# Optimization experiments

Measured on AMD Instinct MI355X. Metric: run time of the kernel, lower is better.

Reference implementation:

```python
import jax, jax.numpy as jnp
import numpy as np
from jax import lax

B, L = 4, 512
D_MODEL, D_STATE, D_CONV, EXPAND = 1024, 16, 4, 2
D_INNER = EXPAND * D_MODEL
DT_RANK = (D_MODEL + 15) // 16  # math.ceil(d_model / 16) = 64


def setup_inputs() -> dict:
    key = jax.random.key(0)
    ks = jax.random.split(key, 16)

    def rn(k, shape, scale=1.0):
        return jax.random.normal(k, shape, jnp.float32) * scale

    # A initialized as log(1..d_state) broadcast over d_inner, as in the module
    A_log = jnp.log(jnp.broadcast_to(jnp.arange(1, D_STATE + 1, dtype=jnp.float32), (D_INNER, D_STATE)))
    return {
        "hidden_states": rn(ks[0], (B, L, D_MODEL)),
        "in_proj_w": rn(ks[1], (2 * D_INNER, D_MODEL), D_MODEL ** -0.5),
        "conv1d_w": rn(ks[2], (D_INNER, 1, D_CONV), D_CONV ** -0.5),
        "conv1d_bias": rn(ks[3], (D_INNER,), 0.02),
        "x_proj_w": rn(ks[4], (DT_RANK + 2 * D_STATE, D_INNER), D_INNER ** -0.5),
        "dt_proj_w": rn(ks[5], (D_INNER, DT_RANK), DT_RANK ** -0.5),
        "dt_proj_bias": rn(ks[6], (D_INNER,), 0.02) - 4.0,
        "A_log": A_log,
        "D": jnp.ones((D_INNER,), jnp.float32),
        "conv1d_b_w": rn(ks[7], (D_INNER, 1, D_CONV), D_CONV ** -0.5),
        "conv1d_b_bias": rn(ks[8], (D_INNER,), 0.02),
        "x_proj_b_w": rn(ks[9], (DT_RANK + 2 * D_STATE, D_INNER), D_INNER ** -0.5),
        "dt_proj_b_w": rn(ks[10], (D_INNER, DT_RANK), DT_RANK ** -0.5),
        "dt_proj_b_bias": rn(ks[11], (D_INNER,), 0.02) - 4.0,
        "A_b_log": A_log,
        "D_b": jnp.ones((D_INNER,), jnp.float32),
        "out_proj_w": rn(ks[12], (D_MODEL, D_INNER), D_INNER ** -0.5),
    }


def _selective_scan(u, delta, A, Bm, Cm, Dv):
    # u, delta: [b,l,d]; Bm, Cm: [b,l,n]; A: [d,n]; Dv: [d]
    # h_t = exp(delta_t * A) * h_{t-1} + delta_t * B_t * u_t ; y_t = <h_t, C_t> + D * u_t
    def step(h, inp):
        u_t, dt_t, B_t, C_t = inp  # [b,d], [b,d], [b,n], [b,n]
        dA = jnp.exp(dt_t[:, :, None] * A)  # [b,d,n]
        h = dA * h + (dt_t * u_t)[:, :, None] * B_t[:, None, :]
        y = jnp.einsum('bdn,bn->bd', h, C_t)
        return h, y

    b, l, d = u.shape
    h0 = jnp.zeros((b, d, A.shape[1]), u.dtype)
    xs = (u.transpose(1, 0, 2), delta.transpose(1, 0, 2), Bm.transpose(1, 0, 2), Cm.transpose(1, 0, 2))
    _, ys = lax.scan(step, h0, xs)  # ys: [l,b,d]
    return ys.transpose(1, 0, 2) + u * Dv


def _direction(x_bdl, conv_w, conv_b, xproj_w, dtproj_w, dtproj_b, A_log, Dv):
    # x_bdl: [b, d_inner, l]. torch pads both sides with d_conv-1 then slices [:L] -> causal depthwise conv.
    xc = lax.conv_general_dilated(x_bdl, conv_w, (1,), [(D_CONV - 1, 0)],
                                  dimension_numbers=('NCH', 'OIH', 'NCH'),
                                  feature_group_count=D_INNER)
    xc = (xc + conv_b[None, :, None]).transpose(0, 2, 1)  # [b,l,d_inner]
    x_dbl = xc @ xproj_w.T  # [b,l,dt_rank+2n]
    dt = x_dbl[..., :DT_RANK] @ dtproj_w.T + dtproj_b
    Bm = x_dbl[..., DT_RANK:DT_RANK + D_STATE]
    Cm = x_dbl[..., DT_RANK + D_STATE:]
    xc = jnp.clip(xc, -10.0, 10.0)
    dt = jnp.clip(dt, 1e-5, 1.0)
    # source passes dt_proj.bias again as delta_bias with delta_softplus=True (bias added twice; faithful)
    delta = jax.nn.softplus(dt + dtproj_b)
    A = -jnp.exp(A_log)
    return _selective_scan(xc, delta, A, Bm, Cm, Dv)


def reference(hidden_states, in_proj_w, conv1d_w, conv1d_bias, x_proj_w, dt_proj_w, dt_proj_bias,
              A_log, D, conv1d_b_w, conv1d_b_bias, x_proj_b_w, dt_proj_b_w, dt_proj_b_bias,
              A_b_log, D_b, out_proj_w):
    xz = (hidden_states @ in_proj_w.T).transpose(0, 2, 1)  # [b, 2*d_inner, l]
    x, z = jnp.split(xz, 2, axis=1)  # each [b, d_inner, l]
    y_fwd = _direction(x, conv1d_w, conv1d_bias, x_proj_w, dt_proj_w, dt_proj_bias, A_log, D)
    y_bwd = _direction(x[:, :, ::-1], conv1d_b_w, conv1d_b_bias, x_proj_b_w, dt_proj_b_w,
                       dt_proj_b_bias, A_b_log, D_b)[:, ::-1, :]  # flip back along seq
    y = (y_fwd + y_bwd) * jax.nn.silu(z.transpose(0, 2, 1))  # [b,l,d_inner]
    out = y @ out_proj_w.T  # [b,l,d_model]
    return jnp.nan_to_num(out, nan=0.0, posinf=1.0, neginf=-1.0)
```

## Files before the change

kernel.cpp:

```cpp
#include <hip/hip_runtime.h>
#include <hip/hip_bf16.h>
#include <math.h>

#define BB 4
#define LL 512
#define DMODEL 1024
#define DSTATE 16
#define DCONV 4
#define DINNER 2048
#define DTRANK 64
#define MROWS (BB*LL)
#define G2KS 4
#define SCHUNK 32
#define SNC (LL / SCHUNK)

typedef __hip_bfloat16 bf16;
typedef __attribute__((ext_vector_type(8))) short short8;
typedef __attribute__((ext_vector_type(4))) short short4v;
typedef __attribute__((ext_vector_type(4))) float f32x4;

__device__ __forceinline__ float softplusf(float x) {
    return x > 20.f ? x : log1pf(__expf(x));
}

__device__ __forceinline__ void stage16(const void* g, void* l) {
    __builtin_amdgcn_global_load_lds(
        (const __attribute__((address_space(1))) void*)g,
        (__attribute__((address_space(3))) void*)l, 16, 0, 0);
}

__device__ __forceinline__ bool a_is_arange(const float* Aa) {
    bool ok = true;
#pragma unroll
    for (int n = 1; n < DSTATE; ++n) {
        float k = (float)(n + 1);
        ok = ok && (fabsf(Aa[n] - k * Aa[0]) <= 1e-4f * k * fabsf(Aa[0]));
    }
    return ok;
}

template<int EPI>
__global__ __launch_bounds__(256) void gemm_bf16(
    const bf16* __restrict__ A, const bf16* __restrict__ W,
    float* __restrict__ C, int N, int K, int lda, int ldw, int ldc)
{
    __shared__ bf16 lA[128 * 32];
    __shared__ bf16 lW[128 * 32];

    const int tid = threadIdx.x;
    const int lane = tid & 63;
    const int wid = tid >> 6;
    const int wr = wid >> 1;
    const int wc = wid & 1;
    const int rowBase = blockIdx.y * 128;
    const int colBase = blockIdx.x * 128;

    const int r16 = lane & 15;
    const int kg = lane >> 4;

    const int srow = (lane >> 2);
    const int scol = (lane & 3) * 8;

    f32x4 acc[4][4];
#pragma unroll
    for (int m = 0; m < 4; ++m)
#pragma unroll
        for (int n = 0; n < 4; ++n) acc[m][n] = (f32x4)0.f;

    for (int k0 = 0; k0 < K; k0 += 32) {
#pragma unroll
        for (int c = 0; c < 2; ++c) {
            int r = wid * 32 + c * 16 + srow;
            stage16(&A[(size_t)(rowBase + r) * lda + k0 + scol],
                    &lA[(wid * 32 + c * 16) * 32]);
            stage16(&W[(size_t)(colBase + r) * ldw + k0 + scol],
                    &lW[(wid * 32 + c * 16) * 32]);
        }
        __syncthreads();

        short8 a[4], b[4];
#pragma unroll
        for (int m = 0; m < 4; ++m)
            a[m] = *(const short8*)&lA[(wr * 64 + m * 16 + r16) * 32 + kg * 8];
#pragma unroll
        for (int n = 0; n < 4; ++n)
            b[n] = *(const short8*)&lW[(wc * 64 + n * 16 + r16) * 32 + kg * 8];
#pragma unroll
        for (int m = 0; m < 4; ++m)
#pragma unroll
            for (int n = 0; n < 4; ++n)
                acc[m][n] = __builtin_amdgcn_mfma_f32_16x16x32_bf16(
                    a[m], b[n], acc[m][n], 0, 0, 0);
        __syncthreads();
    }

#pragma unroll
    for (int m = 0; m < 4; ++m) {
#pragma unroll
        for (int n = 0; n < 4; ++n) {
            int gc = colBase + wc * 64 + n * 16 + r16;
#pragma unroll
            for (int j = 0; j < 4; ++j) {
                int gr = rowBase + wr * 64 + m * 16 + kg * 4 + j;
                float v = acc[m][n][j];
                if (EPI == 2) {
                    if (isnan(v)) v = 0.f;
                    else if (isinf(v)) v = (v > 0.f) ? 1.f : -1.f;
                }
                C[(size_t)gr * ldc + gc] = v;
            }
        }
    }
}

__global__ __launch_bounds__(256) void g4_mfma(
    const bf16* __restrict__ A, const bf16* __restrict__ W,
    float* __restrict__ part)
{
    const int kz = blockIdx.z;
    const int kOff = kz * 1024;
    float* C = part + (size_t)kz * 2048 * 1024;

    __shared__ bf16 lA[128 * 32];
    __shared__ bf16 lW[128 * 32];

    const int tid = threadIdx.x;
    const int lane = tid & 63;
    const int wid = tid >> 6;
    const int wr = wid >> 1;
    const int wc = wid & 1;
    const int rowBase = blockIdx.y * 128;
    const int colBase = blockIdx.x * 128;

    const int r16 = lane & 15;
    const int kg = lane >> 4;
    const int srow = (lane >> 2);
    const int scol = (lane & 3) * 8;

    f32x4 acc[4][4];
#pragma unroll
    for (int m = 0; m < 4; ++m)
#pragma unroll
        for (int n = 0; n < 4; ++n) acc[m][n] = (f32x4)0.f;

    for (int k0 = 0; k0 < 1024; k0 += 32) {
#pragma unroll
        for (int c = 0; c < 2; ++c) {
            int r = wid * 32 + c * 16 + srow;
            stage16(&A[(size_t)(rowBase + r) * 2048 + kOff + k0 + scol],
                    &lA[(wid * 32 + c * 16) * 32]);
            stage16(&W[(size_t)(colBase + r) * 2048 + kOff + k0 + scol],
                    &lW[(wid * 32 + c * 16) * 32]);
        }
        __syncthreads();

        short8 a[4], b[4];
#pragma unroll
        for (int m = 0; m < 4; ++m)
            a[m] = *(const short8*)&lA[(wr * 64 + m * 16 + r16) * 32 + kg * 8];
#pragma unroll
        for (int n = 0; n < 4; ++n)
            b[n] = *(const short8*)&lW[(wc * 64 + n * 16 + r16) * 32 + kg * 8];
#pragma unroll
        for (int m = 0; m < 4; ++m)
#pragma unroll
            for (int n = 0; n < 4; ++n)
                acc[m][n] = __builtin_amdgcn_mfma_f32_16x16x32_bf16(
                    a[m], b[n], acc[m][n], 0, 0, 0);
        __syncthreads();
    }

#pragma unroll
    for (int m = 0; m < 4; ++m) {
#pragma unroll
        for (int n = 0; n < 4; ++n) {
            int gc = colBase + wc * 64 + n * 16 + r16;
#pragma unroll
            for (int j = 0; j < 4; ++j) {
                int gr = rowBase + wr * 64 + m * 16 + kg * 4 + j;
                C[(size_t)gr * 1024 + gc] = acc[m][n][j];
            }
        }
    }
}

__global__ __launch_bounds__(256) void g4_reduce(
    const float* __restrict__ part, float* __restrict__ out)
{
    int i = (blockIdx.x * 256 + threadIdx.x) * 4;
    float4 p0 = *(const float4*)&part[i];
    float4 p1 = *(const float4*)&part[2048 * 1024 + i];
    float r[4] = { p0.x + p1.x, p0.y + p1.y, p0.z + p1.z, p0.w + p1.w };
#pragma unroll
    for (int j = 0; j < 4; ++j) {
        float v = r[j];
        if (isnan(v)) v = 0.f;
        else if (isinf(v)) v = (v > 0.f) ? 1.f : -1.f;
        r[j] = v;
    }
    *(float4*)&out[i] = *(float4*)r;
}

__global__ __launch_bounds__(256) void g3_mfma(
    const bf16* __restrict__ xdbl_bf,
    const bf16* __restrict__ dtw_bf,
    const float* __restrict__ biasf, const float* __restrict__ biasb,
    float* __restrict__ of, float* __restrict__ ob)
{
    const int dir = blockIdx.z;
    const bf16* A = xdbl_bf + (size_t)dir * 2048 * 96;
    const bf16* W = dtw_bf + (size_t)dir * 2048 * 64;
    const float* bias = dir ? biasb : biasf;
    float* C = dir ? ob : of;

    __shared__ bf16 lA[128 * 32];
    __shared__ bf16 lW[128 * 32];

    const int tid = threadIdx.x;
    const int lane = tid & 63;
    const int wid = tid >> 6;
    const int wr = wid >> 1;
    const int wc = wid & 1;
    const int rowBase = blockIdx.y * 128;
    const int colBase = blockIdx.x * 128;

    const int r16 = lane & 15;
    const int kg = lane >> 4;
    const int srow = (lane >> 2);
    const int scol = (lane & 3) * 8;

    f32x4 acc[4][4];
#pragma unroll
    for (int m = 0; m < 4; ++m)
#pragma unroll
        for (int n = 0; n < 4; ++n) acc[m][n] = (f32x4)0.f;

#pragma unroll
    for (int k0 = 0; k0 < 64; k0 += 32) {
#pragma unroll
        for (int c = 0; c < 2; ++c) {
            int r = wid * 32 + c * 16 + srow;
            stage16(&A[(size_t)(rowBase + r) * 96 + k0 + scol],
                    &lA[(wid * 32 + c * 16) * 32]);
            stage16(&W[(size_t)(colBase + r) * 64 + k0 + scol],
                    &lW[(wid * 32 + c * 16) * 32]);
        }
        __syncthreads();

        short8 a[4], b[4];
#pragma unroll
        for (int m = 0; m < 4; ++m)
            a[m] = *(const short8*)&lA[(wr * 64 + m * 16 + r16) * 32 + kg * 8];
#pragma unroll
        for (int n = 0; n < 4; ++n)
            b[n] = *(const short8*)&lW[(wc * 64 + n * 16 + r16) * 32 + kg * 8];
#pragma unroll
        for (int m = 0; m < 4; ++m)
#pragma unroll
            for (int n = 0; n < 4; ++n)
                acc[m][n] = __builtin_amdgcn_mfma_f32_16x16x32_bf16(
                    a[m], b[n], acc[m][n], 0, 0, 0);
        __syncthreads();
    }

#pragma unroll
    for (int m = 0; m < 4; ++m) {
#pragma unroll
        for (int n = 0; n < 4; ++n) {
            int gc = colBase + wc * 64 + n * 16 + r16;
            float bv = bias[gc];
#pragma unroll
            for (int j = 0; j < 4; ++j) {
                int gr = rowBase + wr * 64 + m * 16 + kg * 4 + j;
                float t = acc[m][n][j] + bv;
                t = fminf(fmaxf(t, 1e-5f), 1.0f);
                C[(size_t)gr * 2048 + gc] = softplusf(t + bv);
            }
        }
    }
}

__global__ __launch_bounds__(256) void g2_mfma(
    const bf16* __restrict__ xcbf_f, const bf16* __restrict__ xcbf_b,
    const bf16* __restrict__ wxf, const bf16* __restrict__ wxb,
    float* __restrict__ part)
{
    const int dir = blockIdx.z;
    const bf16* A = dir ? xcbf_b : xcbf_f;
    const bf16* W = dir ? wxb : wxf;
    const int rowBase = blockIdx.x * 128;
    const int kz = blockIdx.y;
    const int kBase = kz * (2048 / G2KS);

    __shared__ bf16 lA[128 * 40];
    __shared__ bf16 lW[96 * 40];

    const int tid = threadIdx.x;
    const int lane = tid & 63;
    const int wid = tid >> 6;
    const int r16 = lane & 15;
    const int kg = lane >> 4;

    f32x4 acc[2][6];
#pragma unroll
    for (int m = 0; m < 2; ++m)
#pragma unroll
        for (int n = 0; n < 6; ++n) acc[m][n] = (f32x4)0.f;

    const int srow = tid >> 2;
    const int scol = (tid & 3) * 8;

    for (int k0 = 0; k0 < 2048 / G2KS; k0 += 32) {
#pragma unroll
        for (int it = 0; it < 2; ++it) {
            int r = srow + it * 64;
            short8 va = *(const short8*)&A[(size_t)(rowBase + r) * 2048 + kBase + k0 + scol];
            *(short8*)&lA[r * 40 + scol] = va;
        }
        {
            short8 vw = *(const short8*)&W[(size_t)srow * 2048 + kBase + k0 + scol];
            *(short8*)&lW[srow * 40 + scol] = vw;
        }
        if (tid < 128) {
            int r = 64 + (tid >> 2);
            short8 vw2 = *(const short8*)&W[(size_t)r * 2048 + kBase + k0 + scol];
            *(short8*)&lW[r * 40 + scol] = vw2;
        }
        __syncthreads();

        short8 a[2], b[6];
#pragma unroll
        for (int m = 0; m < 2; ++m)
            a[m] = *(const short8*)&lA[(wid * 32 + m * 16 + r16) * 40 + kg * 8];
#pragma unroll
        for (int n = 0; n < 6; ++n)
            b[n] = *(const short8*)&lW[(n * 16 + r16) * 40 + kg * 8];
#pragma unroll
        for (int m = 0; m < 2; ++m)
#pragma unroll
            for (int n = 0; n < 6; ++n)
                acc[m][n] = __builtin_amdgcn_mfma_f32_16x16x32_bf16(
                    a[m], b[n], acc[m][n], 0, 0, 0);
        __syncthreads();
    }

    float* p = part + ((size_t)(dir * G2KS + kz) * 2048) * 96;
#pragma unroll
    for (int m = 0; m < 2; ++m) {
#pragma unroll
        for (int n = 0; n < 6; ++n) {
            int gc = n * 16 + r16;
#pragma unroll
            for (int j = 0; j < 4; ++j) {
                int gr = rowBase + wid * 32 + m * 16 + kg * 4 + j;
                p[(size_t)gr * 96 + gc] = acc[m][n][j];
            }
        }
    }
}

__global__ __launch_bounds__(256) void g2_reduce(
    const float* __restrict__ part, float* __restrict__ xf, float* __restrict__ xb,
    bf16* __restrict__ xdbl_bf)
{
    int idx = blockIdx.x * 256 + threadIdx.x;
    int c = idx % 96;
    int r = (idx / 96) & 2047;
    int dir = idx / (96 * 2048);
    float s = 0.f;
#pragma unroll
    for (int ks = 0; ks < G2KS; ++ks)
        s += part[((size_t)(dir * G2KS + ks) * 2048 + r) * 96 + c];
    (dir ? xb : xf)[(size_t)r * 96 + c] = s;
    xdbl_bf[((size_t)dir * 2048 + r) * 96 + c] = __float2bfloat16(s);
}

__global__ __launch_bounds__(256) void cast_all(
    const float* __restrict__ hidden, const float* __restrict__ in_proj_w,
    const float* __restrict__ xproj_w, const float* __restrict__ xproj_bw,
    const float* __restrict__ dtproj_w, const float* __restrict__ dtproj_bw,
    bf16* __restrict__ hbf, bf16* __restrict__ wbf,
    bf16* __restrict__ wxf, bf16* __restrict__ wxb,
    bf16* __restrict__ dtwf, bf16* __restrict__ dtwb)
{
    int bid = blockIdx.x;
    const float* src; bf16* dst; int base;
    if (bid < 1024)      { src = hidden;    dst = hbf;  base = bid; }
    else if (bid < 3072) { src = in_proj_w; dst = wbf;  base = bid - 1024; }
    else if (bid < 3168) { src = xproj_w;   dst = wxf;  base = bid - 3072; }
    else if (bid < 3264) { src = xproj_bw;  dst = wxb;  base = bid - 3168; }
    else if (bid < 3328) { src = dtproj_w;  dst = dtwf; base = bid - 3264; }
    else                 { src = dtproj_bw; dst = dtwb; base = bid - 3328; }
    int i = (base * 256 + threadIdx.x) * 8;
    float4 x = *(const float4*)&src[i];
    float4 y = *(const float4*)&src[i + 4];
    bf16 t[8] = { __float2bfloat16(x.x), __float2bfloat16(x.y),
                  __float2bfloat16(x.z), __float2bfloat16(x.w),
                  __float2bfloat16(y.x), __float2bfloat16(y.y),
                  __float2bfloat16(y.z), __float2bfloat16(y.w) };
    *(short8*)&dst[i] = *(short8*)t;
}

__global__ __launch_bounds__(256) void conv_kernel(
    const float* __restrict__ xz,
    const float* __restrict__ wf, const float* __restrict__ bf,
    const float* __restrict__ wb, const float* __restrict__ bb,
    float* __restrict__ xcf, float* __restrict__ xcb,
    bf16* __restrict__ xcbf, bf16* __restrict__ xcbb)
{
    int idx = blockIdx.x * 256 + threadIdx.x;
    int dg = idx & 511;
    int rest = idx >> 9;
    int l = rest & (LL - 1);
    int b = (rest >> 9) & (BB - 1);
    int dir = rest >> 11;
    int d0 = dg * 4;

    const float* w = dir ? wb : wf;
    const float* bias = dir ? bb : bf;

    float4 wv[4];
#pragma unroll
    for (int c = 0; c < 4; ++c)
        wv[c] = *(const float4*)&w[(d0 + c) * DCONV];

    float4 acc = *(const float4*)&bias[d0];
#pragma unroll
    for (int k = 0; k < DCONV; ++k) {
        int j = l - (DCONV - 1) + k;
        if (j >= 0) {
            int jj = dir ? (LL - 1 - j) : j;
            float4 x = *(const float4*)&xz[((size_t)(b * LL + jj)) * (2 * DINNER) + d0];
            acc.x += ((const float*)&wv[0])[k] * x.x;
            acc.y += ((const float*)&wv[1])[k] * x.y;
            acc.z += ((const float*)&wv[2])[k] * x.z;
            acc.w += ((const float*)&wv[3])[k] * x.w;
        }
    }

    size_t off = ((size_t)(b * LL + l)) * DINNER + d0;
    *(float4*)&((dir ? xcb : xcf)[off]) = acc;
    bf16 t[4] = { __float2bfloat16(acc.x), __float2bfloat16(acc.y),
                  __float2bfloat16(acc.z), __float2bfloat16(acc.w) };
    *(short4v*)&((dir ? xcbb : xcbf)[off]) = *(short4v*)t;
}

__global__ __launch_bounds__(256) void scan1_kernel(
    const float* __restrict__ Alog_f, const float* __restrict__ Alog_b,
    const float* __restrict__ xdbl_f, const float* __restrict__ xdbl_b,
    const float* __restrict__ xc_f, const float* __restrict__ xc_b,
    const float* __restrict__ dl_f, const float* __restrict__ dl_b,
    float* __restrict__ sdel, float* __restrict__ hend)
{
    const int tid = threadIdx.x;
    const int d = blockIdx.x * 256 + tid;
    const int c = blockIdx.y;
    const int z = blockIdx.z;
    const int dir = z >> 2, b = z & 3;

    const float* Alog = dir ? Alog_b : Alog_f;
    const float* xdbl = dir ? xdbl_b : xdbl_f;
    const float* xc   = dir ? xc_b   : xc_f;
    const float* dl   = dir ? dl_b   : dl_f;
    const int rowBase = b * LL + c * SCHUNK;

    __shared__ float bs[SCHUNK][16];
#pragma unroll
    for (int i = 0; i < SCHUNK * 16 / 256; ++i) {
        int e = tid + 256 * i;
        int r = e >> 4, n = e & 15;
        bs[r][n] = xdbl[(size_t)(rowBase + r) * 96 + DTRANK + n];
    }
    __syncthreads();

    float Aa[DSTATE], h[DSTATE];
#pragma unroll
    for (int n = 0; n < DSTATE; ++n) {
        Aa[n] = -__expf(Alog[d * DSTATE + n]);
        h[n] = 0.f;
    }
    float sd = 0.f;
    const bool fast = a_is_arange(Aa);
    const float a0l2 = Aa[0] * 1.44269504f;

    float nxd = dl[(size_t)rowBase * DINNER + d];
    float nxu = xc[(size_t)rowBase * DINNER + d];

    if (fast) {
#pragma unroll 4
        for (int t = 0; t < SCHUNK; ++t) {
            float delta = nxd, u = nxu;
            if (t + 1 < SCHUNK) {
                size_t nrow = (size_t)(rowBase + t + 1);
                nxd = dl[nrow * DINNER + d];
                nxu = xc[nrow * DINNER + d];
            }
            u = fminf(fmaxf(u, -10.f), 10.f);
            float du = delta * u;
            sd += delta;
            float p[DSTATE];
            p[0] = exp2f(delta * a0l2);
#pragma unroll
            for (int n = 1; n < DSTATE; ++n)
                p[n] = p[n >> 1] * p[(n - 1) >> 1];
#pragma unroll
            for (int n = 0; n < DSTATE; ++n)
                h[n] = p[n] * h[n] + du * bs[t][n];
        }
    } else {
#pragma unroll 4
        for (int t = 0; t < SCHUNK; ++t) {
            float delta = nxd, u = nxu;
            if (t + 1 < SCHUNK) {
                size_t nrow = (size_t)(rowBase + t + 1);
                nxd = dl[nrow * DINNER + d];
                nxu = xc[nrow * DINNER + d];
            }
            u = fminf(fmaxf(u, -10.f), 10.f);
            float du = delta * u;
            sd += delta;
#pragma unroll
            for (int n = 0; n < DSTATE; ++n)
                h[n] = __expf(delta * Aa[n]) * h[n] + du * bs[t][n];
        }
    }

    size_t base = (size_t)z * SNC + c;
    sdel[base * DINNER + d] = sd;
#pragma unroll
    for (int n = 0; n < DSTATE; ++n)
        hend[(base * DSTATE + n) * DINNER + d] = h[n];
}

__global__ __launch_bounds__(256) void scan_combine(
    const float* __restrict__ Alog_f, const float* __restrict__ Alog_b,
    const float* __restrict__ sdel, float* __restrict__ hend)
{
    int g = blockIdx.x * 256 + threadIdx.x;
    int d = g & (DINNER - 1);
    int n = (g >> 11) & (DSTATE - 1);
    int z = g >> 15;
    const float* Alog = (z >> 2) ? Alog_b : Alog_f;

    float Aa = -__expf(Alog[d * DSTATE + n]);
    float hr = 0.f;
    for (int c = 0; c < SNC; ++c) {
        size_t base = (size_t)z * SNC + c;
        size_t idx = (base * DSTATE + n) * DINNER + d;
        float he = hend[idx];
        hend[idx] = hr;
        float sd = sdel[base * DINNER + d];
        hr = __expf(sd * Aa) * hr + he;
    }
}

__global__ __launch_bounds__(256) void scan2_kernel(
    const float* __restrict__ Alog_f, const float* __restrict__ Alog_b,
    const float* __restrict__ Df, const float* __restrict__ Db,
    const float* __restrict__ xdbl_f, const float* __restrict__ xdbl_b,
    const float* __restrict__ xc_f, const float* __restrict__ xc_b,
    const float* __restrict__ hin,
    float* __restrict__ dl_f, float* __restrict__ dl_b)
{
    const int tid = threadIdx.x;
    const int d = blockIdx.x * 256 + tid;
    const int c = blockIdx.y;
    const int z = blockIdx.z;
    const int dir = z >> 2, b = z & 3;

    const float* Alog = dir ? Alog_b : Alog_f;
    const float* xdbl = dir ? xdbl_b : xdbl_f;
    const float* xc   = dir ? xc_b   : xc_f;
    float* dl         = dir ? dl_b   : dl_f;
    const int rowBase = b * LL + c * SCHUNK;

    __shared__ float bs[SCHUNK][32];
#pragma unroll
    for (int i = 0; i < SCHUNK * 32 / 256; ++i) {
        int e = tid + 256 * i;
        int r = e >> 5, n = e & 31;
        bs[r][n] = xdbl[(size_t)(rowBase + r) * 96 + DTRANK + n];
    }
    __syncthreads();

    float Dv = (dir ? Db : Df)[d];
    size_t base = (size_t)z * SNC + c;
    float Aa[DSTATE], h[DSTATE];
#pragma unroll
    for (int n = 0; n < DSTATE; ++n) {
        Aa[n] = -__expf(Alog[d * DSTATE + n]);
        h[n] = hin[(base * DSTATE + n) * DINNER + d];
    }
    const bool fast = a_is_arange(Aa);
    const float a0l2 = Aa[0] * 1.44269504f;

    float nxd = dl[(size_t)rowBase * DINNER + d];
    float nxu = xc[(size_t)rowBase * DINNER + d];

    if (fast) {
#pragma unroll 4
        for (int t = 0; t < SCHUNK; ++t) {
            float delta = nxd, u = nxu;
            if (t + 1 < SCHUNK) {
                size_t nrow = (size_t)(rowBase + t + 1);
                nxd = dl[nrow * DINNER + d];
                nxu = xc[nrow * DINNER + d];
            }
            u = fminf(fmaxf(u, -10.f), 10.f);
            float du = delta * u;
            float p[DSTATE];
            p[0] = exp2f(delta * a0l2);
#pragma unroll
            for (int n = 1; n < DSTATE; ++n)
                p[n] = p[n >> 1] * p[(n - 1) >> 1];
            float y = 0.f;
#pragma unroll
            for (int n = 0; n < DSTATE; ++n) {
                h[n] = p[n] * h[n] + du * bs[t][n];
                y += h[n] * bs[t][DSTATE + n];
            }
            dl[(size_t)(rowBase + t) * DINNER + d] = y + u * Dv;
        }
    } else {
#pragma unroll 4
        for (int t = 0; t < SCHUNK; ++t) {
            float delta = nxd, u = nxu;
            if (t + 1 < SCHUNK) {
                size_t nrow = (size_t)(rowBase + t + 1);
                nxd = dl[nrow * DINNER + d];
                nxu = xc[nrow * DINNER + d];
            }
            u = fminf(fmaxf(u, -10.f), 10.f);
            float du = delta * u;
            float y = 0.f;
#pragma unroll
            for (int n = 0; n < DSTATE; ++n) {
                h[n] = __expf(delta * Aa[n]) * h[n] + du * bs[t][n];
                y += h[n] * bs[t][DSTATE + n];
            }
            dl[(size_t)(rowBase + t) * DINNER + d] = y + u * Dv;
        }
    }
}

__global__ __launch_bounds__(256) void gate_cast(
    const float* __restrict__ yf, const float* __restrict__ yb,
    const float* __restrict__ xz, bf16* __restrict__ ytot,
    const float* __restrict__ out_pw, bf16* __restrict__ obf)
{
    int bid = blockIdx.x;
    if (bid < 16384) {
        int idx = bid * 256 + threadIdx.x;
        int d = idx & (DINNER - 1);
        int l = (idx >> 11) & (LL - 1);
        int b = idx >> 20;
        size_t rowf = (size_t)(b * LL + l);
        size_t rowb = (size_t)(b * LL + (LL - 1 - l));
        float y = yf[rowf * DINNER + d] + yb[rowb * DINNER + d];
        float z = xz[rowf * (2 * DINNER) + DINNER + d];
        float s = z / (1.f + __expf(-z));
        ytot[rowf * DINNER + d] = __float2bfloat16(y * s);
    } else {
        int i = ((bid - 16384) * 256 + threadIdx.x) * 8;
        float4 x = *(const float4*)&out_pw[i];
        float4 y = *(const float4*)&out_pw[i + 4];
        bf16 t[8] = { __float2bfloat16(x.x), __float2bfloat16(x.y),
                      __float2bfloat16(x.z), __float2bfloat16(x.w),
                      __float2bfloat16(y.x), __float2bfloat16(y.y),
                      __float2bfloat16(y.z), __float2bfloat16(y.w) };
        *(short8*)&obf[i] = *(short8*)t;
    }
}

extern "C" void kernel_launch(void* const* d_in, const int* in_sizes, int n_in,
                              void* d_out, int out_size, void* d_ws, size_t ws_size,
                              hipStream_t stream)
{
    const float* hidden    = (const float*)d_in[0];
    const float* in_proj_w = (const float*)d_in[1];
    const float* conv_w    = (const float*)d_in[2];
    const float* conv_b    = (const float*)d_in[3];
    const float* xproj_w   = (const float*)d_in[4];
    const float* dtproj_w  = (const float*)d_in[5];
    const float* dtproj_b  = (const float*)d_in[6];
    const float* A_log     = (const float*)d_in[7];
    const float* Dvec      = (const float*)d_in[8];
    const float* conv_bw   = (const float*)d_in[9];
    const float* conv_bb   = (const float*)d_in[10];
    const float* xproj_bw  = (const float*)d_in[11];
    const float* dtproj_bw = (const float*)d_in[12];
    const float* dtproj_bb = (const float*)d_in[13];
    const float* A_b_log   = (const float*)d_in[14];
    const float* D_b       = (const float*)d_in[15];
    const float* out_pw    = (const float*)d_in[16];
    float* out = (float*)d_out;

    float* ws = (float*)d_ws;
    float* xz      = ws;
    float* xc_f    = xz + 8388608;
    float* xc_b    = xc_f + 4194304;
    float* xdbl_f  = xc_b + 4194304;
    float* xdbl_b  = xdbl_f + 196608;
    float* dl_f    = xdbl_b + 196608;
    float* dl_b    = dl_f + 4194304;
    float* g2part  = dl_b + 4194304;
    float* sdel    = g2part + 1572864;
    float* hend    = sdel + 262144;
    float* smallb  = hend + 4194304;

    bf16* hbf = (bf16*)dl_f;
    bf16* wbf = (bf16*)(dl_f + 1048576);
    bf16* wxf = (bf16*)dl_b;
    bf16* wxb = (bf16*)(dl_b + 98304);
    bf16* xcbf = (bf16*)hend;
    bf16* xcbb = (bf16*)(hend + 2097152);
    bf16* xdbl_bf = (bf16*)smallb;
    bf16* dtw_bf  = (bf16*)(smallb + 196608);
    bf16* ytot_bf = (bf16*)xc_f;
    bf16* obf = (bf16*)xc_b;
    float* g4part = dl_f;

    dim3 blk(256);

    cast_all<<<dim3(3392), blk, 0, stream>>>(
        hidden, in_proj_w, xproj_w, xproj_bw, dtproj_w, dtproj_bw,
        hbf, wbf, wxf, wxb, dtw_bf, dtw_bf + 131072);

    gemm_bf16<0><<<dim3(4096 / 128, MROWS / 128), blk, 0, stream>>>(
        hbf, wbf, xz, 4096, 1024, 1024, 1024, 4096);

    conv_kernel<<<dim3(2 * BB * LL * DINNER / 4 / 256), blk, 0, stream>>>(
        xz, conv_w, conv_b, conv_bw, conv_bb, xc_f, xc_b, xcbf, xcbb);

    g2_mfma<<<dim3(16, G2KS, 2), blk, 0, stream>>>(
        xcbf, xcbb, wxf, wxb, g2part);
    g2_reduce<<<dim3(2 * 2048 * 96 / 256), blk, 0, stream>>>(
        g2part, xdbl_f, xdbl_b, xdbl_bf);

    g3_mfma<<<dim3(16, 16, 2), blk, 0, stream>>>(
        xdbl_bf, dtw_bf, dtproj_b, dtproj_bb, dl_f, dl_b);

    scan1_kernel<<<dim3(DINNER / 256, SNC, 8), blk, 0, stream>>>(
        A_log, A_b_log, xdbl_f, xdbl_b, xc_f, xc_b, dl_f, dl_b, sdel, hend);
    scan_combine<<<dim3(2 * BB * DSTATE * DINNER / 256), blk, 0, stream>>>(
        A_log, A_b_log, sdel, hend);
    scan2_kernel<<<dim3(DINNER / 256, SNC, 8), blk, 0, stream>>>(
        A_log, A_b_log, Dvec, D_b, xdbl_f, xdbl_b, xc_f, xc_b, hend, dl_f, dl_b);

    gate_cast<<<dim3(16384 + 1024), blk, 0, stream>>>(
        dl_f, dl_b, xz, ytot_bf, out_pw, obf);

    g4_mfma<<<dim3(1024 / 128, MROWS / 128, 2), blk, 0, stream>>>(
        ytot_bf, obf, g4part);
    g4_reduce<<<dim3(2048 * 1024 / 4 / 256), blk, 0, stream>>>(g4part, out);
}
```

Before: 224.9 us.

## Store conv output, delta and scan outputs as bf16 to cut memory traffic

The conv kernel now writes only the bf16 copy of its output, and the scan kernels read that bf16 copy instead of an fp32 one. The dt projection writes delta as bf16, and scan2 writes y as bf16 in place, which gate_cast then reads. This halves the bytes moved through the memory-bound conv, scan and gating stages and drops a redundant fp32 store. The workspace aliases are reworked so the bf16 buffers reuse the old fp32 regions. The cost is bf16 rounding of delta, u and y, which may loosen accuracy.

```diff
diff --git a/kernel.cpp b/kernel.cpp
--- a/kernel.cpp
+++ b/kernel.cpp
@@ -57,7 +57,6 @@
 
     const int r16 = lane & 15;
     const int kg = lane >> 4;
-
     const int srow = (lane >> 2);
     const int scol = (lane & 3) * 8;
 
@@ -205,13 +204,13 @@
     const bf16* __restrict__ xdbl_bf,
     const bf16* __restrict__ dtw_bf,
     const float* __restrict__ biasf, const float* __restrict__ biasb,
-    float* __restrict__ of, float* __restrict__ ob)
+    bf16* __restrict__ of, bf16* __restrict__ ob)
 {
     const int dir = blockIdx.z;
     const bf16* A = xdbl_bf + (size_t)dir * 2048 * 96;
     const bf16* W = dtw_bf + (size_t)dir * 2048 * 64;
     const float* bias = dir ? biasb : biasf;
-    float* C = dir ? ob : of;
+    bf16* C = dir ? ob : of;
 
     __shared__ bf16 lA[128 * 32];
     __shared__ bf16 lW[128 * 32];
@@ -274,7 +273,7 @@
                 int gr = rowBase + wr * 64 + m * 16 + kg * 4 + j;
                 float t = acc[m][n][j] + bv;
                 t = fminf(fmaxf(t, 1e-5f), 1.0f);
-                C[(size_t)gr * 2048 + gc] = softplusf(t + bv);
+                C[(size_t)gr * 2048 + gc] = __float2bfloat16(softplusf(t + bv));
             }
         }
     }
@@ -405,7 +404,6 @@
     const float* __restrict__ xz,
     const float* __restrict__ wf, const float* __restrict__ bf,
     const float* __restrict__ wb, const float* __restrict__ bb,
-    float* __restrict__ xcf, float* __restrict__ xcb,
     bf16* __restrict__ xcbf, bf16* __restrict__ xcbb)
 {
     int idx = blockIdx.x * 256 + threadIdx.x;
@@ -439,7 +437,6 @@
     }
 
     size_t off = ((size_t)(b * LL + l)) * DINNER + d0;
-    *(float4*)&((dir ? xcb : xcf)[off]) = acc;
     bf16 t[4] = { __float2bfloat16(acc.x), __float2bfloat16(acc.y),
                   __float2bfloat16(acc.z), __float2bfloat16(acc.w) };
     *(short4v*)&((dir ? xcbb : xcbf)[off]) = *(short4v*)t;
@@ -448,8 +445,8 @@
 __global__ __launch_bounds__(256) void scan1_kernel(
     const float* __restrict__ Alog_f, const float* __restrict__ Alog_b,
     const float* __restrict__ xdbl_f, const float* __restrict__ xdbl_b,
-    const float* __restrict__ xc_f, const float* __restrict__ xc_b,
-    const float* __restrict__ dl_f, const float* __restrict__ dl_b,
+    const bf16* __restrict__ xc_f, const bf16* __restrict__ xc_b,
+    const bf16* __restrict__ dl_f, const bf16* __restrict__ dl_b,
     float* __restrict__ sdel, float* __restrict__ hend)
 {
     const int tid = threadIdx.x;
@@ -460,8 +457,8 @@
 
     const float* Alog = dir ? Alog_b : Alog_f;
     const float* xdbl = dir ? xdbl_b : xdbl_f;
-    const float* xc   = dir ? xc_b   : xc_f;
-    const float* dl   = dir ? dl_b   : dl_f;
+    const bf16* xc    = dir ? xc_b   : xc_f;
+    const bf16* dl    = dir ? dl_b   : dl_f;
     const int rowBase = b * LL + c * SCHUNK;
 
     __shared__ float bs[SCHUNK][16];
@@ -483,8 +480,8 @@
     const bool fast = a_is_arange(Aa);
     const float a0l2 = Aa[0] * 1.44269504f;
 
-    float nxd = dl[(size_t)rowBase * DINNER + d];
-    float nxu = xc[(size_t)rowBase * DINNER + d];
+    float nxd = __bfloat162float(dl[(size_t)rowBase * DINNER + d]);
+    float nxu = __bfloat162float(xc[(size_t)rowBase * DINNER + d]);
 
     if (fast) {
 #pragma unroll 4
@@ -492,8 +489,8 @@
             float delta = nxd, u = nxu;
             if (t + 1 < SCHUNK) {
                 size_t nrow = (size_t)(rowBase + t + 1);
-                nxd = dl[nrow * DINNER + d];
-                nxu = xc[nrow * DINNER + d];
+                nxd = __bfloat162float(dl[nrow * DINNER + d]);
+                nxu = __bfloat162float(xc[nrow * DINNER + d]);
             }
             u = fminf(fmaxf(u, -10.f), 10.f);
             float du = delta * u;
@@ -513,8 +510,8 @@
             float delta = nxd, u = nxu;
             if (t + 1 < SCHUNK) {
                 size_t nrow = (size_t)(rowBase + t + 1);
-                nxd = dl[nrow * DINNER + d];
-                nxu = xc[nrow * DINNER + d];
+                nxd = __bfloat162float(dl[nrow * DINNER + d]);
+                nxu = __bfloat162float(xc[nrow * DINNER + d]);
             }
             u = fminf(fmaxf(u, -10.f), 10.f);
             float du = delta * u;
@@ -558,9 +555,9 @@
     const float* __restrict__ Alog_f, const float* __restrict__ Alog_b,
     const float* __restrict__ Df, const float* __restrict__ Db,
     const float* __restrict__ xdbl_f, const float* __restrict__ xdbl_b,
-    const float* __restrict__ xc_f, const float* __restrict__ xc_b,
+    const bf16* __restrict__ xc_f, const bf16* __restrict__ xc_b,
     const float* __restrict__ hin,
-    float* __restrict__ dl_f, float* __restrict__ dl_b)
+    bf16* __restrict__ dl_f, bf16* __restrict__ dl_b)
 {
     const int tid = threadIdx.x;
     const int d = blockIdx.x * 256 + tid;
@@ -570,8 +567,8 @@
 
     const float* Alog = dir ? Alog_b : Alog_f;
     const float* xdbl = dir ? xdbl_b : xdbl_f;
-    const float* xc   = dir ? xc_b   : xc_f;
-    float* dl         = dir ? dl_b   : dl_f;
+    const bf16* xc    = dir ? xc_b   : xc_f;
+    bf16* dl          = dir ? dl_b   : dl_f;
     const int rowBase = b * LL + c * SCHUNK;
 
     __shared__ float bs[SCHUNK][32];
@@ -594,8 +591,8 @@
     const bool fast = a_is_arange(Aa);
     const float a0l2 = Aa[0] * 1.44269504f;
 
-    float nxd = dl[(size_t)rowBase * DINNER + d];
-    float nxu = xc[(size_t)rowBase * DINNER + d];
+    float nxd = __bfloat162float(dl[(size_t)rowBase * DINNER + d]);
+    float nxu = __bfloat162float(xc[(size_t)rowBase * DINNER + d]);
 
     if (fast) {
 #pragma unroll 4
@@ -603,8 +600,8 @@
             float delta = nxd, u = nxu;
             if (t + 1 < SCHUNK) {
                 size_t nrow = (size_t)(rowBase + t + 1);
-                nxd = dl[nrow * DINNER + d];
-                nxu = xc[nrow * DINNER + d];
+                nxd = __bfloat162float(dl[nrow * DINNER + d]);
+                nxu = __bfloat162float(xc[nrow * DINNER + d]);
             }
             u = fminf(fmaxf(u, -10.f), 10.f);
             float du = delta * u;
@@ -619,7 +616,7 @@
                 h[n] = p[n] * h[n] + du * bs[t][n];
                 y += h[n] * bs[t][DSTATE + n];
             }
-            dl[(size_t)(rowBase + t) * DINNER + d] = y + u * Dv;
+            dl[(size_t)(rowBase + t) * DINNER + d] = __float2bfloat16(y + u * Dv);
         }
     } else {
 #pragma unroll 4
@@ -627,8 +624,8 @@
             float delta = nxd, u = nxu;
             if (t + 1 < SCHUNK) {
                 size_t nrow = (size_t)(rowBase + t + 1);
-                nxd = dl[nrow * DINNER + d];
-                nxu = xc[nrow * DINNER + d];
+                nxd = __bfloat162float(dl[nrow * DINNER + d]);
+                nxu = __bfloat162float(xc[nrow * DINNER + d]);
             }
             u = fminf(fmaxf(u, -10.f), 10.f);
             float du = delta * u;
@@ -638,13 +635,13 @@
                 h[n] = __expf(delta * Aa[n]) * h[n] + du * bs[t][n];
                 y += h[n] * bs[t][DSTATE + n];
             }
-            dl[(size_t)(rowBase + t) * DINNER + d] = y + u * Dv;
+            dl[(size_t)(rowBase + t) * DINNER + d] = __float2bfloat16(y + u * Dv);
         }
     }
 }
 
 __global__ __launch_bounds__(256) void gate_cast(
-    const float* __restrict__ yf, const float* __restrict__ yb,
+    const bf16* __restrict__ yf, const bf16* __restrict__ yb,
     const float* __restrict__ xz, bf16* __restrict__ ytot,
     const float* __restrict__ out_pw, bf16* __restrict__ obf)
 {
@@ -656,7 +653,8 @@
         int b = idx >> 20;
         size_t rowf = (size_t)(b * LL + l);
         size_t rowb = (size_t)(b * LL + (LL - 1 - l));
-        float y = yf[rowf * DINNER + d] + yb[rowb * DINNER + d];
+        float y = __bfloat162float(yf[rowf * DINNER + d]) +
+                  __bfloat162float(yb[rowb * DINNER + d]);
         float z = xz[rowf * (2 * DINNER) + DINNER + d];
         float s = z / (1.f + __expf(-z));
         ytot[rowf * DINNER + d] = __float2bfloat16(y * s);
@@ -697,28 +695,30 @@
 
     float* ws = (float*)d_ws;
     float* xz      = ws;
-    float* xc_f    = xz + 8388608;
-    float* xc_b    = xc_f + 4194304;
-    float* xdbl_f  = xc_b + 4194304;
+    float* xcR_f   = xz + 8388608;
+    float* xcR_b   = xcR_f + 4194304;
+    float* xdbl_f  = xcR_b + 4194304;
     float* xdbl_b  = xdbl_f + 196608;
-    float* dl_f    = xdbl_b + 196608;
-    float* dl_b    = dl_f + 4194304;
-    float* g2part  = dl_b + 4194304;
+    float* dlR_f   = xdbl_b + 196608;
+    float* dlR_b   = dlR_f + 4194304;
+    float* g2part  = dlR_b + 4194304;
     float* sdel    = g2part + 1572864;
     float* hend    = sdel + 262144;
     float* smallb  = hend + 4194304;
 
-    bf16* hbf = (bf16*)dl_f;
-    bf16* wbf = (bf16*)(dl_f + 1048576);
-    bf16* wxf = (bf16*)dl_b;
-    bf16* wxb = (bf16*)(dl_b + 98304);
-    bf16* xcbf = (bf16*)hend;
-    bf16* xcbb = (bf16*)(hend + 2097152);
+    bf16* xcbf = (bf16*)xcR_f;
+    bf16* xcbb = (bf16*)xcR_b;
+    bf16* dlbf_f = (bf16*)dlR_f;
+    bf16* dlbf_b = (bf16*)dlR_b;
+    bf16* hbf = (bf16*)dlR_f;
+    bf16* wbf = (bf16*)(dlR_f + 1048576);
+    bf16* wxf = (bf16*)dlR_b;
+    bf16* wxb = (bf16*)(dlR_b + 98304);
     bf16* xdbl_bf = (bf16*)smallb;
     bf16* dtw_bf  = (bf16*)(smallb + 196608);
-    bf16* ytot_bf = (bf16*)xc_f;
-    bf16* obf = (bf16*)xc_b;
-    float* g4part = dl_f;
+    bf16* ytot_bf = (bf16*)xcR_f;
+    bf16* obf = (bf16*)xcR_b;
+    float* g4part = dlR_f;
 
     dim3 blk(256);
 
@@ -730,7 +730,7 @@
         hbf, wbf, xz, 4096, 1024, 1024, 1024, 4096);
 
     conv_kernel<<<dim3(2 * BB * LL * DINNER / 4 / 256), blk, 0, stream>>>(
-        xz, conv_w, conv_b, conv_bw, conv_bb, xc_f, xc_b, xcbf, xcbb);
+        xz, conv_w, conv_b, conv_bw, conv_bb, xcbf, xcbb);
 
     g2_mfma<<<dim3(16, G2KS, 2), blk, 0, stream>>>(
         xcbf, xcbb, wxf, wxb, g2part);
@@ -738,17 +738,17 @@
         g2part, xdbl_f, xdbl_b, xdbl_bf);
 
     g3_mfma<<<dim3(16, 16, 2), blk, 0, stream>>>(
-        xdbl_bf, dtw_bf, dtproj_b, dtproj_bb, dl_f, dl_b);
+        xdbl_bf, dtw_bf, dtproj_b, dtproj_bb, dlbf_f, dlbf_b);
 
     scan1_kernel<<<dim3(DINNER / 256, SNC, 8), blk, 0, stream>>>(
-        A_log, A_b_log, xdbl_f, xdbl_b, xc_f, xc_b, dl_f, dl_b, sdel, hend);
+        A_log, A_b_log, xdbl_f, xdbl_b, xcbf, xcbb, dlbf_f, dlbf_b, sdel, hend);
     scan_combine<<<dim3(2 * BB * DSTATE * DINNER / 256), blk, 0, stream>>>(
         A_log, A_b_log, sdel, hend);
     scan2_kernel<<<dim3(DINNER / 256, SNC, 8), blk, 0, stream>>>(
-        A_log, A_b_log, Dvec, D_b, xdbl_f, xdbl_b, xc_f, xc_b, hend, dl_f, dl_b);
+        A_log, A_b_log, Dvec, D_b, xdbl_f, xdbl_b, xcbf, xcbb, hend, dlbf_f, dlbf_b);
 
     gate_cast<<<dim3(16384 + 1024), blk, 0, stream>>>(
-        dl_f, dl_b, xz, ytot_bf, out_pw, obf);
+        dlbf_f, dlbf_b, xz, ytot_bf, out_pw, obf);
 
     g4_mfma<<<dim3(1024 / 128, MROWS / 128, 2), blk, 0, stream>>>(
         ytot_bf, obf, g4part);
```

Result: faster. 219.3 us (-2.5%).
